# Optimization experiments

Measured on AMD Instinct MI355X. Metric: run time of the kernel, lower is better.

The kernel has to match this reference:

```python
import jax, jax.numpy as jnp
import numpy as np

B, N, D, H, DH = 64, 512, 128, 4, 32  # graphs, nodes/graph, emb_dim, heads, head_dim
E = 8192  # edges per graph (avg degree 16)


def setup_inputs() -> dict:
    key = jax.random.key(0)
    ks = jax.random.split(key, 12)
    total_nodes = B * N
    # within-graph random edges, then shift to global node ids
    src = jax.random.randint(ks[0], (B, E), 0, N)
    dst = jax.random.randint(ks[1], (B, E), 0, N)
    offs = (jnp.arange(B) * N)[:, None]
    edge_index = jnp.stack([(src + offs).reshape(-1), (dst + offs).reshape(-1)], axis=0)
    batch = jnp.repeat(jnp.arange(B), N)
    inner = H * DH
    s = lambda d: 1.0 / np.sqrt(d)
    return {
        "x": jax.random.normal(ks[2], (total_nodes, D), jnp.float32),
        "edge_index": edge_index,
        "edge_embedding": jax.random.normal(ks[3], (B * E, D), jnp.float32),
        "batch": batch,
        "W_gcn": jax.random.normal(ks[4], (D, D), jnp.float32) * s(D),
        "b_gcn": jnp.zeros((D,), jnp.float32),
        "root_emb": jax.random.normal(ks[5], (1, D), jnp.float32),
        "Wq": jax.random.normal(ks[6], (D, inner), jnp.float32) * s(D),
        "Wkv": jax.random.normal(ks[7], (D, 2 * inner), jnp.float32) * s(D),
        "Wout": jax.random.normal(ks[8], (inner, D), jnp.float32) * s(inner),
        "b_out": jnp.zeros((D,), jnp.float32),
    }


def reference(x, edge_index, edge_embedding, batch, W_gcn, b_gcn, root_emb, Wq, Wkv, Wout, b_out):
    total_nodes = x.shape[0]
    row, col = edge_index[0], edge_index[1]
    # ---- GCNConv ----
    h = x @ W_gcn + b_gcn
    deg = jax.ops.segment_sum(jnp.ones_like(row, dtype=h.dtype), row, num_segments=total_nodes) + 1.0
    dinv = deg ** -0.5  # deg >= 1, no inf
    norm = dinv[row] * dinv[col]
    msg = norm[:, None] * jax.nn.relu(h[row] + edge_embedding)
    agg = jax.ops.segment_sum(msg, col, num_segments=total_nodes)
    h = agg + jax.nn.relu(h + root_emb) / deg[:, None]
    # ---- dense batch (uniform graph sizes -> reshape) + masked self-attention ----
    nf = h.reshape(B, N, D)
    q = (nf @ Wq).reshape(B, N, H, DH)
    kv = nf @ Wkv
    k = kv[..., : H * DH].reshape(B, N, H, DH)
    v = kv[..., H * DH :].reshape(B, N, H, DH)
    scale = DH ** -0.5
    sim = jnp.einsum("bihd,bjhd->bhij", q, k) * scale
    attn = jax.nn.softmax(sim, axis=-1)  # all-true node mask (uniform batches)
    out = jnp.einsum("bhij,bjhd->bihd", attn, v).reshape(B, N, H * DH)
    out = out @ Wout + b_out
    return out.reshape(total_nodes, D)
```

## Files before the change

### kernel.cpp

```cpp
#include <hip/hip_runtime.h>
#include <hip/hip_bf16.h>

#define TOTAL_NODES 32768
#define NNODE 512
#define ETOT 524288

typedef unsigned short u16;
typedef __attribute__((ext_vector_type(8))) short bf16x8;
typedef __attribute__((ext_vector_type(4))) float f32x4;

union U8 { bf16x8 v; u16 s[8]; uint4 q; };

__device__ __forceinline__ float bf2f(u16 u) {
    union { unsigned int i; float f; } x; x.i = ((unsigned int)u) << 16; return x.f;
}
__device__ __forceinline__ u16 f2bf(float f) {
    union { __hip_bfloat16 h; u16 u; } c; c.h = __float2bfloat16(f); return c.u;
}
__device__ __forceinline__ f32x4 mfma16(bf16x8 a, bf16x8 b, f32x4 c) {
    return __builtin_amdgcn_mfma_f32_16x16x32_bf16(a, b, c, 0, 0, 0);
}

__global__ void hist_kernel(const int* __restrict__ ei, int* __restrict__ cnt_row,
                            int* __restrict__ cnt_col) {
    int e = blockIdx.x * blockDim.x + threadIdx.x;
    if (e < ETOT) {
        atomicAdd(&cnt_row[ei[e]], 1);
        atomicAdd(&cnt_col[ei[ETOT + e]], 1);
    }
}

__global__ __launch_bounds__(1024) void scan_kernel(const int* __restrict__ cnt,
                                                    int* __restrict__ offs,
                                                    int* __restrict__ cur,
                                                    const int* __restrict__ cnt_row,
                                                    float* __restrict__ dinv) {
    __shared__ int part[1024];
    const int t = threadIdx.x;
    const int base = t * 32;
    int local[32];
    int s = 0;
#pragma unroll
    for (int i = 0; i < 32; i++) { local[i] = s; s += cnt[base + i]; }
    part[t] = s;
    __syncthreads();
    for (int off = 1; off < 1024; off <<= 1) {
        int v = (t >= off) ? part[t - off] : 0;
        __syncthreads();
        part[t] += v;
        __syncthreads();
    }
    int prefix = (t == 0) ? 0 : part[t - 1];
#pragma unroll
    for (int i = 0; i < 32; i++) {
        int o = prefix + local[i];
        offs[base + i] = o;
        cur[base + i] = o;
    }
    if (t == 1023) offs[32768] = prefix + s;
#pragma unroll
    for (int i = 0; i < 32; i++)
        dinv[base + i] = rsqrtf((float)cnt_row[base + i] + 1.0f);
}

__global__ void scatter_kernel(const int* __restrict__ ei, int* __restrict__ cur,
                               int2* __restrict__ pairs) {
    int e = blockIdx.x * blockDim.x + threadIdx.x;
    if (e < ETOT) {
        int r = ei[e], c = ei[ETOT + e];
        int pos = atomicAdd(&cur[c], 1);
        pairs[pos] = make_int2(r, e);
    }
}

__global__ __launch_bounds__(128) void gather_kernel(const int2* __restrict__ pairs,
                                                     const int* __restrict__ offs,
                                                     const int* __restrict__ cnt_row,
                                                     const float* __restrict__ dinv,
                                                     const float* __restrict__ h0,
                                                     const float* __restrict__ ee,
                                                     const float* __restrict__ root,
                                                     float* __restrict__ h) {
    const int c = blockIdx.x;
    const int d = threadIdx.x;
    const int s = offs[c], e_end = offs[c + 1];
    float acc = 0.0f;
    int i = s;
    for (; i + 2 <= e_end; i += 2) {
        int2 p0 = pairs[i], p1 = pairs[i + 1];
        float d0 = dinv[p0.x], d1 = dinv[p1.x];
        float v0 = h0[(size_t)p0.x * 128 + d] + ee[(size_t)p0.y * 128 + d];
        float v1 = h0[(size_t)p1.x * 128 + d] + ee[(size_t)p1.y * 128 + d];
        acc += fmaxf(v0, 0.0f) * d0 + fmaxf(v1, 0.0f) * d1;
    }
    for (; i < e_end; i++) {
        int2 p0 = pairs[i];
        float v0 = h0[(size_t)p0.x * 128 + d] + ee[(size_t)p0.y * 128 + d];
        acc += fmaxf(v0, 0.0f) * dinv[p0.x];
    }
    float degc = (float)cnt_row[c] + 1.0f;
    float hv = h0[(size_t)c * 128 + d] + root[d];
    h[(size_t)c * 128 + d] = dinv[c] * acc + fmaxf(hv, 0.0f) / degc;
}

template <int OUTC>
__global__ __launch_bounds__(256) void gemm_kernel(const float* __restrict__ in,
                                                   const float* __restrict__ W,
                                                   const float* __restrict__ bias,
                                                   float* __restrict__ outp) {
    __shared__ __align__(16) float a_lds[8 * 128];
    const int rb = blockIdx.x * 8;
    const int t = threadIdx.x;
    for (int idx = t; idx < 8 * 128; idx += OUTC)
        a_lds[idx] = in[(size_t)(rb + (idx >> 7)) * 128 + (idx & 127)];
    __syncthreads();

    float acc[8];
    float bv = bias ? bias[t] : 0.0f;
#pragma unroll
    for (int r = 0; r < 8; r++) acc[r] = bv;

    const float4* a4 = (const float4*)a_lds;
    for (int k4 = 0; k4 < 32; k4++) {
        float w0 = W[(k4 * 4 + 0) * OUTC + t];
        float w1 = W[(k4 * 4 + 1) * OUTC + t];
        float w2 = W[(k4 * 4 + 2) * OUTC + t];
        float w3 = W[(k4 * 4 + 3) * OUTC + t];
#pragma unroll
        for (int r = 0; r < 8; r++) {
            float4 a = a4[r * 32 + k4];
            acc[r] = fmaf(a.x, w0, fmaf(a.y, w1, fmaf(a.z, w2, fmaf(a.w, w3, acc[r]))));
        }
    }
#pragma unroll
    for (int r = 0; r < 8; r++) outp[(size_t)(rb + r) * OUTC + t] = acc[r];
}

__global__ __launch_bounds__(384) void qkv_kernel(const float* __restrict__ in,
                                                  const float* __restrict__ Wq,
                                                  const float* __restrict__ Wkv,
                                                  float* __restrict__ qout,
                                                  u16* __restrict__ khi,
                                                  u16* __restrict__ klo,
                                                  u16* __restrict__ vT) {
    __shared__ __align__(16) float a_lds[8 * 128];
    __shared__ __align__(16) u16 kstage[2][8 * 128];
    const int rb = blockIdx.x * 8;
    const int t = threadIdx.x;
    for (int idx = t; idx < 8 * 128; idx += 384)
        a_lds[idx] = in[(size_t)(rb + (idx >> 7)) * 128 + (idx & 127)];
    __syncthreads();

    float acc[8];
#pragma unroll
    for (int r = 0; r < 8; r++) acc[r] = 0.0f;

    const float4* a4 = (const float4*)a_lds;
    const bool isq = (t < 128);
    const float* Wp = isq ? (Wq + t) : (Wkv + (t - 128));
    const int ldw = isq ? 128 : 256;
    for (int k4 = 0; k4 < 32; k4++) {
        float w0 = Wp[(size_t)(k4 * 4 + 0) * ldw];
        float w1 = Wp[(size_t)(k4 * 4 + 1) * ldw];
        float w2 = Wp[(size_t)(k4 * 4 + 2) * ldw];
        float w3 = Wp[(size_t)(k4 * 4 + 3) * ldw];
#pragma unroll
        for (int r = 0; r < 8; r++) {
            float4 a = a4[r * 32 + k4];
            acc[r] = fmaf(a.x, w0, fmaf(a.y, w1, fmaf(a.z, w2, fmaf(a.w, w3, acc[r]))));
        }
    }

    const int b = rb >> 9;
    const int rbl = rb & 511;

    if (t < 128) {
#pragma unroll
        for (int r = 0; r < 8; r++) qout[(size_t)(rb + r) * 128 + t] = acc[r];
    } else if (t < 256) {
        const int c = t - 128;
#pragma unroll
        for (int r = 0; r < 8; r++) {
            u16 hi = f2bf(acc[r]);
            kstage[0][r * 128 + c] = hi;
            kstage[1][r * 128 + c] = f2bf(acc[r] - bf2f(hi));
        }
    } else {
        const int c = t - 256;
        const int h = c >> 5, d = c & 31;
        const int bh = b * 4 + h;
        U8 u;
#pragma unroll
        for (int r = 0; r < 8; r++) u.s[r] = f2bf(acc[r]);
        *(uint4*)(vT + ((size_t)(bh * 64 + (rbl >> 3)) * 32 + d) * 8) = u.q;
    }
    __syncthreads();
    if (t < 256) {
        const int hl = t >> 7;
        const int u = t & 127;
        const int h = u >> 5;
        const int j = u & 31;
        const int n = j >> 2, dq = j & 3;
        uint4 val = *(const uint4*)(&kstage[hl][n * 128 + h * 32 + dq * 8]);
        u16* dst = (hl ? klo : khi) + (size_t)(b * 4 + h) * 16384 + (size_t)(rbl + n) * 32 + dq * 8;
        *(uint4*)dst = val;
    }
}

__global__ __launch_bounds__(256) void attn_mfma_kernel(const float* __restrict__ qbuf,
                                                        const u16* __restrict__ khi,
                                                        const u16* __restrict__ klo,
                                                        const u16* __restrict__ vT,
                                                        float* __restrict__ ao) {
    __shared__ u16 transit[8][16 * 36];
    const int t = threadIdx.x;
    const int w = t >> 6, L = t & 63;
    const int n16 = L & 15, quad = L >> 4;
    const int bh = blockIdx.y, b = bh >> 2, h = bh & 3;
    const int qbase = blockIdx.x * 128 + w * 32;

    bf16x8 qhi[2], qlo[2];
#pragma unroll
    for (int p = 0; p < 2; p++) {
        const float* qp = qbuf + (size_t)(b * 512 + qbase + p * 16 + n16) * 128 + h * 32 + quad * 8;
        U8 uh, ul;
#pragma unroll
        for (int j = 0; j < 8; j++) {
            float f = qp[j] * 0.17677669529663687f;
            u16 hi = f2bf(f);
            uh.s[j] = hi;
            ul.s[j] = f2bf(f - bf2f(hi));
        }
        qhi[p] = uh.v; qlo[p] = ul.v;
    }

    const f32x4 zero = {0.f, 0.f, 0.f, 0.f};

    float m[2][4];
#pragma unroll
    for (int p = 0; p < 2; p++)
#pragma unroll
        for (int r = 0; r < 4; r++) m[p][r] = -1e30f;

    for (int j0 = 0; j0 < 512; j0 += 16) {
        U8 ub; ub.q = *(const uint4*)(khi + (size_t)(bh * 512 + j0 + n16) * 32 + quad * 8);
#pragma unroll
        for (int p = 0; p < 2; p++) {
            f32x4 s = mfma16(qhi[p], ub.v, zero);
#pragma unroll
            for (int r = 0; r < 4; r++) m[p][r] = fmaxf(m[p][r], s[r]);
        }
    }
#pragma unroll
    for (int p = 0; p < 2; p++)
#pragma unroll
        for (int r = 0; r < 4; r++) {
            float mv = m[p][r];
#pragma unroll
            for (int mask = 1; mask < 16; mask <<= 1) mv = fmaxf(mv, __shfl_xor(mv, mask));
            m[p][r] = mv;
        }

    float l[2][4] = {{0.f, 0.f, 0.f, 0.f}, {0.f, 0.f, 0.f, 0.f}};
    f32x4 O[2][2];
#pragma unroll
    for (int p = 0; p < 2; p++)
#pragma unroll
        for (int dt = 0; dt < 2; dt++) O[p][dt] = zero;

    u16* tr[2] = { transit[w * 2 + 0], transit[w * 2 + 1] };

    for (int jb = 0; jb < 512; jb += 32) {
#pragma unroll
        for (int jt = 0; jt < 2; jt++) {
            const int j0 = jb + jt * 16;
            const size_t kidx = (size_t)(bh * 512 + j0 + n16) * 32 + quad * 8;
            U8 uh; uh.q = *(const uint4*)(khi + kidx);
            U8 ul; ul.q = *(const uint4*)(klo + kidx);
#pragma unroll
            for (int p = 0; p < 2; p++) {
                f32x4 s = mfma16(qhi[p], uh.v, zero);
                s = mfma16(qhi[p], ul.v, s);
                s = mfma16(qlo[p], uh.v, s);
#pragma unroll
                for (int r = 0; r < 4; r++) {
                    float pr = __expf(s[r] - m[p][r]);
                    u16 pb = f2bf(pr);
                    l[p][r] += bf2f(pb);
                    tr[p][(quad * 4 + r) * 36 + jt * 16 + n16] = pb;
                }
            }
        }
        bf16x8 A[2];
#pragma unroll
        for (int p = 0; p < 2; p++) {
            const u16* trp = tr[p];
            const int off = n16 * 36 + quad * 8;
            uint2 lo = *(const uint2*)(trp + off);
            uint2 hi2 = *(const uint2*)(trp + off + 4);
            U8 ua; ua.q = make_uint4(lo.x, lo.y, hi2.x, hi2.y);
            A[p] = ua.v;
        }
#pragma unroll
        for (int dt = 0; dt < 2; dt++) {
            U8 uv; uv.q = *(const uint4*)(vT + (size_t)bh * 16384
                                          + (size_t)((jb + quad * 8) >> 3) * 256
                                          + (size_t)(dt * 16 + n16) * 8);
#pragma unroll
            for (int p = 0; p < 2; p++) O[p][dt] = mfma16(A[p], uv.v, O[p][dt]);
        }
    }

#pragma unroll
    for (int p = 0; p < 2; p++)
#pragma unroll
        for (int r = 0; r < 4; r++) {
            float lv = l[p][r];
#pragma unroll
            for (int mask = 1; mask < 16; mask <<= 1) lv += __shfl_xor(lv, mask);
            float inv = 1.0f / lv;
#pragma unroll
            for (int dt = 0; dt < 2; dt++)
                ao[(size_t)(b * 512 + qbase + p * 16 + quad * 4 + r) * 128 + h * 32 + dt * 16 + n16]
                    = O[p][dt][r] * inv;
        }
}

extern "C" void kernel_launch(void* const* d_in, const int* in_sizes, int n_in,
                              void* d_out, int out_size, void* d_ws, size_t ws_size,
                              hipStream_t stream) {
    const float* x    = (const float*)d_in[0];
    const int*   ei   = (const int*)d_in[1];
    const float* ee   = (const float*)d_in[2];
    const float* Wg   = (const float*)d_in[4];
    const float* bg   = (const float*)d_in[5];
    const float* root = (const float*)d_in[6];
    const float* Wq   = (const float*)d_in[7];
    const float* Wkv  = (const float*)d_in[8];
    const float* Wo   = (const float*)d_in[9];
    const float* bo   = (const float*)d_in[10];

    char* ws = (char*)d_ws;
    int*   cnt_row = (int*)ws;
    float* dinv    = (float*)(ws + 131072);
    float* buf1    = (float*)(ws + 262144);
    float* hbuf    = buf1 + 4194304;
    char*  reg3    = (char*)(hbuf + 4194304);
    u16*   khi     = (u16*)reg3;
    u16*   klo     = khi + 4194304;
    u16*   vT      = (u16*)d_out;
    int*   cnt_col = (int*)reg3;
    int*   offs    = cnt_col + 32768;
    int*   cur     = offs + 32769;
    int2*  pairs   = (int2*)(cur + 32768 + 1023);

    hipMemsetAsync(cnt_row, 0, 131072, stream);
    hipMemsetAsync(cnt_col, 0, 131072, stream);

    hist_kernel<<<2048, 256, 0, stream>>>(ei, cnt_row, cnt_col);
    scan_kernel<<<1, 1024, 0, stream>>>(cnt_col, offs, cur, cnt_row, dinv);
    scatter_kernel<<<2048, 256, 0, stream>>>(ei, cur, pairs);

    gemm_kernel<128><<<4096, 128, 0, stream>>>(x, Wg, bg, buf1);

    gather_kernel<<<32768, 128, 0, stream>>>(pairs, offs, cnt_row, dinv, buf1, ee, root, hbuf);

    qkv_kernel<<<4096, 384, 0, stream>>>(hbuf, Wq, Wkv, buf1, khi, klo, vT);

    attn_mfma_kernel<<<dim3(4, 256), 256, 0, stream>>>(buf1, khi, klo, vT, buf1);

    gemm_kernel<128><<<4096, 128, 0, stream>>>(buf1, Wo, bo, (float*)d_out);
}
```

Baseline: 646.1 us.

## Replace FP32 SIMT GEMMs with split-bf16 MFMA GEMMs and pre-transposed weights

Adds a weight prep kernel that transposes all weight matrices and splits each into bf16 hi/lo parts. The GCN, QKV and output projections become MFMA kernels over 64-row tiles, using three MFMAs per k-step to approximate fp32 precision. The aim is to move the dense projections off scalar FMA onto matrix cores and cut per-block redundant weight reads. The cost is an extra launch, slight precision loss, and scalar 2-byte K stores in place of the earlier staged vector stores.

```diff
diff --git a/kernel.cpp b/kernel.cpp
--- a/kernel.cpp
+++ b/kernel.cpp
@@ -103,107 +103,159 @@
     h[(size_t)c * 128 + d] = dinv[c] * acc + fmaxf(hv, 0.0f) / degc;
 }
 
-template <int OUTC>
-__global__ __launch_bounds__(256) void gemm_kernel(const float* __restrict__ in,
-                                                   const float* __restrict__ W,
-                                                   const float* __restrict__ bias,
-                                                   float* __restrict__ outp) {
-    __shared__ __align__(16) float a_lds[8 * 128];
-    const int rb = blockIdx.x * 8;
+__global__ __launch_bounds__(256) void wprep_kernel(const float* __restrict__ Wg,
+                                                    const float* __restrict__ Wq,
+                                                    const float* __restrict__ Wkv,
+                                                    const float* __restrict__ Wo,
+                                                    u16* __restrict__ wt) {
+    int idx = blockIdx.x * 256 + threadIdx.x;
+    const float* W; int outc; int local; u16* hi; u16* lo;
+    if (idx < 16384)      { W = Wg;  outc = 128; local = idx;         hi = wt;          lo = wt + 16384; }
+    else if (idx < 32768) { W = Wq;  outc = 128; local = idx - 16384; hi = wt + 32768;  lo = wt + 49152; }
+    else if (idx < 65536) { W = Wkv; outc = 256; local = idx - 32768; hi = wt + 65536;  lo = wt + 98304; }
+    else                  { W = Wo;  outc = 128; local = idx - 65536; hi = wt + 131072; lo = wt + 147456; }
+    int c = local >> 7, k = local & 127;
+    float f = W[(size_t)k * outc + c];
+    u16 h = f2bf(f);
+    hi[local] = h;
+    lo[local] = f2bf(f - bf2f(h));
+}
+
+__global__ __launch_bounds__(256) void mgemm_kernel(const float* __restrict__ in,
+                                                    const u16* __restrict__ wthi,
+                                                    const u16* __restrict__ wtlo,
+                                                    const float* __restrict__ bias,
+                                                    float* __restrict__ outp) {
+    __shared__ __align__(16) u16 ahi[64 * 136];
+    __shared__ __align__(16) u16 alo[64 * 136];
     const int t = threadIdx.x;
-    for (int idx = t; idx < 8 * 128; idx += OUTC)
-        a_lds[idx] = in[(size_t)(rb + (idx >> 7)) * 128 + (idx & 127)];
+    const int rb = blockIdx.x * 64;
+    for (int i = t; i < 8192; i += 256) {
+        int r = i >> 7, k = i & 127;
+        float f = in[(size_t)(rb + r) * 128 + k];
+        u16 h = f2bf(f);
+        ahi[r * 136 + k] = h;
+        alo[r * 136 + k] = f2bf(f - bf2f(h));
+    }
     __syncthreads();
-
-    float acc[8];
-    float bv = bias ? bias[t] : 0.0f;
-#pragma unroll
-    for (int r = 0; r < 8; r++) acc[r] = bv;
-
-    const float4* a4 = (const float4*)a_lds;
-    for (int k4 = 0; k4 < 32; k4++) {
-        float w0 = W[(k4 * 4 + 0) * OUTC + t];
-        float w1 = W[(k4 * 4 + 1) * OUTC + t];
-        float w2 = W[(k4 * 4 + 2) * OUTC + t];
-        float w3 = W[(k4 * 4 + 3) * OUTC + t];
-#pragma unroll
-        for (int r = 0; r < 8; r++) {
-            float4 a = a4[r * 32 + k4];
-            acc[r] = fmaf(a.x, w0, fmaf(a.y, w1, fmaf(a.z, w2, fmaf(a.w, w3, acc[r]))));
-        }
-    }
-#pragma unroll
-    for (int r = 0; r < 8; r++) outp[(size_t)(rb + r) * OUTC + t] = acc[r];
-}
-
-__global__ __launch_bounds__(384) void qkv_kernel(const float* __restrict__ in,
-                                                  const float* __restrict__ Wq,
-                                                  const float* __restrict__ Wkv,
-                                                  float* __restrict__ qout,
-                                                  u16* __restrict__ khi,
-                                                  u16* __restrict__ klo,
-                                                  u16* __restrict__ vT) {
-    __shared__ __align__(16) float a_lds[8 * 128];
-    __shared__ __align__(16) u16 kstage[2][8 * 128];
-    const int rb = blockIdx.x * 8;
+    const int w = t >> 6, L = t & 63, n16 = L & 15, quad = L >> 4;
+    const int row0 = w * 16;
+    bf16x8 Ah[4], Al[4];
+#pragma unroll
+    for (int kt = 0; kt < 4; kt++) {
+        Ah[kt] = *(const bf16x8*)(ahi + (row0 + n16) * 136 + kt * 32 + quad * 8);
+        Al[kt] = *(const bf16x8*)(alo + (row0 + n16) * 136 + kt * 32 + quad * 8);
+    }
+    const f32x4 zero = {0.f, 0.f, 0.f, 0.f};
+#pragma unroll
+    for (int ct = 0; ct < 8; ct++) {
+        f32x4 acc = zero;
+#pragma unroll
+        for (int kt = 0; kt < 4; kt++) {
+            U8 bh_, bl_;
+            bh_.q = *(const uint4*)(wthi + (ct * 16 + n16) * 128 + kt * 32 + quad * 8);
+            bl_.q = *(const uint4*)(wtlo + (ct * 16 + n16) * 128 + kt * 32 + quad * 8);
+            acc = mfma16(Ah[kt], bh_.v, acc);
+            acc = mfma16(Ah[kt], bl_.v, acc);
+            acc = mfma16(Al[kt], bh_.v, acc);
+        }
+        float bv = bias ? bias[ct * 16 + n16] : 0.0f;
+#pragma unroll
+        for (int r = 0; r < 4; r++)
+            outp[(size_t)(rb + row0 + quad * 4 + r) * 128 + ct * 16 + n16] = acc[r] + bv;
+    }
+}
+
+__global__ __launch_bounds__(256) void qkv_mfma_kernel(const float* __restrict__ in,
+                                                       const u16* __restrict__ wt,
+                                                       float* __restrict__ qout,
+                                                       u16* __restrict__ khi,
+                                                       u16* __restrict__ klo,
+                                                       u16* __restrict__ vT) {
+    __shared__ __align__(16) u16 ahi[64 * 136];
+    __shared__ __align__(16) u16 alo[64 * 136];
     const int t = threadIdx.x;
-    for (int idx = t; idx < 8 * 128; idx += 384)
-        a_lds[idx] = in[(size_t)(rb + (idx >> 7)) * 128 + (idx & 127)];
+    const int rb = blockIdx.x * 64;
+    for (int i = t; i < 8192; i += 256) {
+        int r = i >> 7, k = i & 127;
+        float f = in[(size_t)(rb + r) * 128 + k];
+        u16 h = f2bf(f);
+        ahi[r * 136 + k] = h;
+        alo[r * 136 + k] = f2bf(f - bf2f(h));
+    }
     __syncthreads();
-
-    float acc[8];
-#pragma unroll
-    for (int r = 0; r < 8; r++) acc[r] = 0.0f;
-
-    const float4* a4 = (const float4*)a_lds;
-    const bool isq = (t < 128);
-    const float* Wp = isq ? (Wq + t) : (Wkv + (t - 128));
-    const int ldw = isq ? 128 : 256;
-    for (int k4 = 0; k4 < 32; k4++) {
-        float w0 = Wp[(size_t)(k4 * 4 + 0) * ldw];
-        float w1 = Wp[(size_t)(k4 * 4 + 1) * ldw];
-        float w2 = Wp[(size_t)(k4 * 4 + 2) * ldw];
-        float w3 = Wp[(size_t)(k4 * 4 + 3) * ldw];
-#pragma unroll
-        for (int r = 0; r < 8; r++) {
-            float4 a = a4[r * 32 + k4];
-            acc[r] = fmaf(a.x, w0, fmaf(a.y, w1, fmaf(a.z, w2, fmaf(a.w, w3, acc[r]))));
-        }
-    }
-
-    const int b = rb >> 9;
-    const int rbl = rb & 511;
-
-    if (t < 128) {
-#pragma unroll
-        for (int r = 0; r < 8; r++) qout[(size_t)(rb + r) * 128 + t] = acc[r];
-    } else if (t < 256) {
-        const int c = t - 128;
-#pragma unroll
-        for (int r = 0; r < 8; r++) {
-            u16 hi = f2bf(acc[r]);
-            kstage[0][r * 128 + c] = hi;
-            kstage[1][r * 128 + c] = f2bf(acc[r] - bf2f(hi));
-        }
-    } else {
-        const int c = t - 256;
-        const int h = c >> 5, d = c & 31;
-        const int bh = b * 4 + h;
-        U8 u;
-#pragma unroll
-        for (int r = 0; r < 8; r++) u.s[r] = f2bf(acc[r]);
-        *(uint4*)(vT + ((size_t)(bh * 64 + (rbl >> 3)) * 32 + d) * 8) = u.q;
-    }
-    __syncthreads();
-    if (t < 256) {
-        const int hl = t >> 7;
-        const int u = t & 127;
-        const int h = u >> 5;
-        const int j = u & 31;
-        const int n = j >> 2, dq = j & 3;
-        uint4 val = *(const uint4*)(&kstage[hl][n * 128 + h * 32 + dq * 8]);
-        u16* dst = (hl ? klo : khi) + (size_t)(b * 4 + h) * 16384 + (size_t)(rbl + n) * 32 + dq * 8;
-        *(uint4*)dst = val;
+    const int w = t >> 6, L = t & 63, n16 = L & 15, quad = L >> 4;
+    const int row0 = w * 16;
+    const int b = rb >> 9, rbl = rb & 511;
+    bf16x8 Ah[4], Al[4];
+#pragma unroll
+    for (int kt = 0; kt < 4; kt++) {
+        Ah[kt] = *(const bf16x8*)(ahi + (row0 + n16) * 136 + kt * 32 + quad * 8);
+        Al[kt] = *(const bf16x8*)(alo + (row0 + n16) * 136 + kt * 32 + quad * 8);
+    }
+    const f32x4 zero = {0.f, 0.f, 0.f, 0.f};
+    const u16* WqT_hi  = wt + 32768;
+    const u16* WqT_lo  = wt + 49152;
+    const u16* WkvT_hi = wt + 65536;
+    const u16* WkvT_lo = wt + 98304;
+
+#pragma unroll
+    for (int ct = 0; ct < 8; ct++) {
+        f32x4 acc = zero;
+#pragma unroll
+        for (int kt = 0; kt < 4; kt++) {
+            U8 bh_, bl_;
+            bh_.q = *(const uint4*)(WqT_hi + (ct * 16 + n16) * 128 + kt * 32 + quad * 8);
+            bl_.q = *(const uint4*)(WqT_lo + (ct * 16 + n16) * 128 + kt * 32 + quad * 8);
+            acc = mfma16(Ah[kt], bh_.v, acc);
+            acc = mfma16(Ah[kt], bl_.v, acc);
+            acc = mfma16(Al[kt], bh_.v, acc);
+        }
+#pragma unroll
+        for (int r = 0; r < 4; r++)
+            qout[(size_t)(rb + row0 + quad * 4 + r) * 128 + ct * 16 + n16] = acc[r];
+    }
+
+#pragma unroll
+    for (int ct = 0; ct < 8; ct++) {
+        f32x4 acc = zero;
+#pragma unroll
+        for (int kt = 0; kt < 4; kt++) {
+            U8 bh_, bl_;
+            bh_.q = *(const uint4*)(WkvT_hi + (ct * 16 + n16) * 128 + kt * 32 + quad * 8);
+            bl_.q = *(const uint4*)(WkvT_lo + (ct * 16 + n16) * 128 + kt * 32 + quad * 8);
+            acc = mfma16(Ah[kt], bh_.v, acc);
+            acc = mfma16(Ah[kt], bl_.v, acc);
+            acc = mfma16(Al[kt], bh_.v, acc);
+        }
+        const int c = ct * 16 + n16, hh = c >> 5, d = c & 31;
+        const size_t base = ((size_t)(b * 4 + hh) * 512 + (rbl + row0 + quad * 4)) * 32 + d;
+#pragma unroll
+        for (int r = 0; r < 4; r++) {
+            u16 hv = f2bf(acc[r]);
+            khi[base + (size_t)r * 32] = hv;
+            klo[base + (size_t)r * 32] = f2bf(acc[r] - bf2f(hv));
+        }
+    }
+
+#pragma unroll
+    for (int ct = 0; ct < 8; ct++) {
+        f32x4 acc = zero;
+#pragma unroll
+        for (int kt = 0; kt < 4; kt++) {
+            U8 bh_, bl_;
+            bh_.q = *(const uint4*)(WkvT_hi + (128 + ct * 16 + n16) * 128 + kt * 32 + quad * 8);
+            bl_.q = *(const uint4*)(WkvT_lo + (128 + ct * 16 + n16) * 128 + kt * 32 + quad * 8);
+            acc = mfma16(Ah[kt], bh_.v, acc);
+            acc = mfma16(Ah[kt], bl_.v, acc);
+            acc = mfma16(Al[kt], bh_.v, acc);
+        }
+        const int c = ct * 16 + n16, hh = c >> 5, d = c & 31;
+        const int n0 = rbl + row0 + quad * 4;
+        unsigned int w0 = (unsigned int)f2bf(acc[0]) | ((unsigned int)f2bf(acc[1]) << 16);
+        unsigned int w1 = (unsigned int)f2bf(acc[2]) | ((unsigned int)f2bf(acc[3]) << 16);
+        uint2 val = make_uint2(w0, w1);
+        *(uint2*)(vT + (size_t)(b * 4 + hh) * 16384 + (size_t)(n0 >> 3) * 256 + d * 8 + (n0 & 7)) = val;
     }
 }
 
@@ -348,6 +400,7 @@
     char*  reg3    = (char*)(hbuf + 4194304);
     u16*   khi     = (u16*)reg3;
     u16*   klo     = khi + 4194304;
+    u16*   wt      = (u16*)(reg3 + 16777216);
     u16*   vT      = (u16*)d_out;
     int*   cnt_col = (int*)reg3;
     int*   offs    = cnt_col + 32768;
@@ -357,17 +410,19 @@
     hipMemsetAsync(cnt_row, 0, 131072, stream);
     hipMemsetAsync(cnt_col, 0, 131072, stream);
 
+    wprep_kernel<<<320, 256, 0, stream>>>(Wg, Wq, Wkv, Wo, wt);
+
     hist_kernel<<<2048, 256, 0, stream>>>(ei, cnt_row, cnt_col);
     scan_kernel<<<1, 1024, 0, stream>>>(cnt_col, offs, cur, cnt_row, dinv);
     scatter_kernel<<<2048, 256, 0, stream>>>(ei, cur, pairs);
 
-    gemm_kernel<128><<<4096, 128, 0, stream>>>(x, Wg, bg, buf1);
+    mgemm_kernel<<<512, 256, 0, stream>>>(x, wt, wt + 16384, bg, buf1);
 
     gather_kernel<<<32768, 128, 0, stream>>>(pairs, offs, cnt_row, dinv, buf1, ee, root, hbuf);
 
-    qkv_kernel<<<4096, 384, 0, stream>>>(hbuf, Wq, Wkv, buf1, khi, klo, vT);
+    qkv_mfma_kernel<<<512, 256, 0, stream>>>(hbuf, wt, buf1, khi, klo, vT);
 
     attn_mfma_kernel<<<dim3(4, 256), 256, 0, stream>>>(buf1, khi, klo, vT, buf1);
 
-    gemm_kernel<128><<<4096, 128, 0, stream>>>(buf1, Wo, bo, (float*)d_out);
-}
+    mgemm_kernel<<<512, 256, 0, stream>>>(buf1, wt + 131072, wt + 147456, bo, (float*)d_out);
+}
```

Result: faster. 608.6 us (-5.8%).
